# Performance work log

Measured on AMD Instinct MI355X. Metric: run time of the kernel, lower is better.

The kernel has to match this reference:

```python
import math
import jax, jax.numpy as jnp
import numpy as np

N_HEAD = 1
NORM_GROUPS = 32
EPS = 1e-5


def setup_inputs() -> dict:
    key = jax.random.key(0)
    ks = jax.random.split(key, 3)
    B, C, H, W, L = 4, 64, 16, 16, 16
    x = jax.random.normal(ks[0], (B, C, H, W, L), dtype=jnp.float32)
    gn_weight = jnp.ones((C,), dtype=jnp.float32)
    gn_bias = jnp.zeros((C,), dtype=jnp.float32)
    # 1x1x1 conv == per-voxel matmul; init like torch conv (kaiming-ish scale)
    qkv_weight = jax.random.normal(ks[1], (3 * C, C), dtype=jnp.float32) / math.sqrt(C)
    out_weight = jax.random.normal(ks[2], (C, C), dtype=jnp.float32) / math.sqrt(C)
    out_bias = jnp.zeros((C,), dtype=jnp.float32)
    return {"x": x, "gn_weight": gn_weight, "gn_bias": gn_bias,
            "qkv_weight": qkv_weight, "out_weight": out_weight, "out_bias": out_bias}


def _group_norm(x, w, b):
    B, C, H, W, L = x.shape
    g = NORM_GROUPS
    xg = x.reshape(B, g, C // g, H, W, L)
    mean = xg.mean(axis=(2, 3, 4, 5), keepdims=True)
    var = xg.var(axis=(2, 3, 4, 5), keepdims=True)
    xn = ((xg - mean) * jax.lax.rsqrt(var + EPS)).reshape(B, C, H, W, L)
    return xn * w[None, :, None, None, None] + b[None, :, None, None, None]


def reference(x, gn_weight, gn_bias, qkv_weight, out_weight, out_bias):
    B, C, H, W, L = x.shape
    n_head = N_HEAD
    head_dim = C // n_head
    N = H * W * L  # flattened voxel count

    norm = _group_norm(x, gn_weight, gn_bias)
    # 1x1x1 conv C -> 3C (no bias), then split heads
    qkv = jnp.einsum('bchwl,dc->bdhwl', norm, qkv_weight)
    qkv = qkv.reshape(B, n_head, 3 * head_dim, N)
    q, k, v = jnp.split(qkv, 3, axis=2)  # each [B, n_head, head_dim, N]

    # full N^2 attention; scale by sqrt(channel) as in the original (NOT head_dim)
    attn = jnp.einsum('bncq,bnck->bnqk', q, k) / math.sqrt(C)
    attn = jax.nn.softmax(attn, axis=-1)
    out = jnp.einsum('bnqk,bnck->bncq', attn, v).reshape(B, C, H, W, L)

    out = jnp.einsum('bchwl,dc->bdhwl', out, out_weight) + out_bias[None, :, None, None, None]
    return out + x
```

## Files before the change

### kernel.cpp

```cpp
#include <hip/hip_runtime.h>
#include <hip/hip_bf16.h>
#include <math.h>

#define BATCH 4
#define CH    64
#define NVOX  4096
#define NGRP  32
#define EPS   1e-5f
#define SPLITS 4
#define KVS   (NVOX / SPLITS)

typedef float f32x4 __attribute__((ext_vector_type(4)));
typedef short s16x8 __attribute__((ext_vector_type(8)));

static __device__ inline unsigned short f2bf(float f) {
    union { __hip_bfloat16 h; unsigned short u; } cv;
    cv.h = __float2bfloat16(f);
    return cv.u;
}

__global__ __launch_bounds__(256) void k_gnstats(const float* __restrict__ x,
                                                 float* __restrict__ stats) {
    int bg = blockIdx.x;
    const float4* p4 = (const float4*)(x + (size_t)bg * (2 * NVOX));
    float s = 0.f, sq = 0.f;
    for (int i = threadIdx.x; i < (2 * NVOX) / 4; i += 256) {
        float4 v = p4[i];
        s  += v.x + v.y + v.z + v.w;
        sq += v.x * v.x + v.y * v.y + v.z * v.z + v.w * v.w;
    }
    for (int off = 32; off; off >>= 1) {
        s  += __shfl_down(s, off);
        sq += __shfl_down(sq, off);
    }
    __shared__ float ls[4], lq[4];
    int wid = threadIdx.x >> 6;
    if ((threadIdx.x & 63) == 0) { ls[wid] = s; lq[wid] = sq; }
    __syncthreads();
    if (threadIdx.x == 0) {
        s  = ls[0] + ls[1] + ls[2] + ls[3];
        sq = lq[0] + lq[1] + lq[2] + lq[3];
        float mean = s / (float)(2 * NVOX);
        float var  = sq / (float)(2 * NVOX) - mean * mean;
        stats[bg]       = mean;
        stats[128 + bg] = rsqrtf(var + EPS);
    }
}

__global__ __launch_bounds__(256) void k_qkv(const float* __restrict__ x,
                                             const float* __restrict__ stats,
                                             const float* __restrict__ gw,
                                             const float* __restrict__ gb,
                                             const float* __restrict__ W,
                                             unsigned short* __restrict__ Qb,
                                             unsigned short* __restrict__ Kb,
                                             unsigned short* __restrict__ Vb) {
    int b  = blockIdx.x >> 6;
    int n0 = (blockIdx.x & 63) * 64;
    int t  = threadIdx.x;
    __shared__ float nm[64][64];
    __shared__ alignas(16) unsigned short tb[64][72];

    for (int i = t; i < 64 * 16; i += 256) {
        int c = i >> 4;
        int n = (i & 15) * 4;
        float4 v = *(const float4*)&x[((size_t)(b * CH + c)) * NVOX + n0 + n];
        float mean = stats[b * NGRP + (c >> 1)];
        float rstd = stats[128 + b * NGRP + (c >> 1)];
        float sc = rstd * gw[c];
        float sh = gb[c] - mean * sc;
        nm[c][n + 0] = v.x * sc + sh;
        nm[c][n + 1] = v.y * sc + sh;
        nm[c][n + 2] = v.z * sc + sh;
        nm[c][n + 3] = v.w * sc + sh;
    }
    __syncthreads();

    int nl = t & 63;
    int dg = t >> 6;
    float r[64];
    #pragma unroll
    for (int c = 0; c < 64; ++c) r[c] = nm[c][nl];

    #pragma unroll 4
    for (int j = 0; j < 16; ++j) {
        int d = dg * 16 + j;
        const float* w = &W[d * 64];
        float acc = 0.f;
        #pragma unroll
        for (int c = 0; c < 64; ++c) acc += w[c] * r[c];
        tb[nl][d] = f2bf(acc * 0.125f);
    }
    __syncthreads();
    {
        int n = t >> 2, d0 = (t & 3) * 16;
        s16x8 a0 = *(const s16x8*)&tb[n][d0];
        s16x8 a1 = *(const s16x8*)&tb[n][d0 + 8];
        size_t base = ((size_t)(b * NVOX + n0 + n)) * 64 + d0;
        *(s16x8*)&Qb[base]     = a0;
        *(s16x8*)&Qb[base + 8] = a1;
    }
    __syncthreads();

    #pragma unroll 4
    for (int j = 0; j < 16; ++j) {
        int d = dg * 16 + j;
        const float* w = &W[(64 + d) * 64];
        float acc = 0.f;
        #pragma unroll
        for (int c = 0; c < 64; ++c) acc += w[c] * r[c];
        tb[nl][d] = f2bf(acc);
    }
    __syncthreads();
    {
        int n = t >> 2, d0 = (t & 3) * 16;
        s16x8 a0 = *(const s16x8*)&tb[n][d0];
        s16x8 a1 = *(const s16x8*)&tb[n][d0 + 8];
        size_t base = ((size_t)(b * NVOX + n0 + n)) * 64 + d0;
        *(s16x8*)&Kb[base]     = a0;
        *(s16x8*)&Kb[base + 8] = a1;
    }

    #pragma unroll 4
    for (int j = 0; j < 16; ++j) {
        int d = dg * 16 + j;
        const float* w = &W[(128 + d) * 64];
        float acc = 0.f;
        #pragma unroll
        for (int c = 0; c < 64; ++c) acc += w[c] * r[c];
        Vb[((size_t)(b * 64 + d)) * NVOX + n0 + nl] = f2bf(acc);
    }
}

__global__ __launch_bounds__(256) void k_attn(const unsigned short* __restrict__ Qb,
                                              const unsigned short* __restrict__ Kb,
                                              const unsigned short* __restrict__ Vb,
                                              float* __restrict__ Opart,
                                              float* __restrict__ Mpart,
                                              float* __restrict__ Lpart) {
    int split = blockIdx.x & 3;
    int bq    = blockIdx.x >> 2;
    int b     = bq >> 6;
    int q0    = (bq & 63) * 64;
    int t     = threadIdx.x;
    int lane  = t & 63;
    int w     = t >> 6;
    const int kbase = split * KVS;

    __shared__ alignas(16) unsigned short Ks[64][72];
    __shared__ alignas(16) unsigned short Vs[64][72];
    __shared__ alignas(16) unsigned short Ps[4][16][72];

    const unsigned short* Qp = Qb + (size_t)b * NVOX * 64;
    const unsigned short* Kp = Kb + (size_t)b * NVOX * 64;
    const unsigned short* Vp = Vb + (size_t)b * 64 * NVOX;

    int l15 = lane & 15;
    int g4  = lane >> 4;
    int csl = g4 * 8;
    int qrow = q0 + w * 16 + l15;
    s16x8 qf0 = *(const s16x8*)&Qp[(size_t)qrow * 64 + csl];
    s16x8 qf1 = *(const s16x8*)&Qp[(size_t)qrow * 64 + csl + 32];

    f32x4 acc_o[4] = {};
    float m_r[4], l_r[4];
    #pragma unroll
    for (int i = 0; i < 4; ++i) { m_r[i] = -1e30f; l_r[i] = 0.f; }

    int sr = t >> 2;
    int sc = (t & 3) * 16;

    s16x8 kr0, kr1, vr0, vr1;
    {
        const s16x8* pk = (const s16x8*)&Kp[((size_t)(kbase + sr)) * 64 + sc];
        kr0 = pk[0]; kr1 = pk[1];
        const s16x8* pv = (const s16x8*)&Vp[(size_t)sr * NVOX + kbase + sc];
        vr0 = pv[0]; vr1 = pv[1];
    }

    for (int it = 0; it < KVS / 64; ++it) {
        *(s16x8*)&Ks[sr][sc]     = kr0;
        *(s16x8*)&Ks[sr][sc + 8] = kr1;
        *(s16x8*)&Vs[sr][sc]     = vr0;
        *(s16x8*)&Vs[sr][sc + 8] = vr1;
        __syncthreads();

        if (it < KVS / 64 - 1) {
            int k0n = kbase + (it + 1) * 64;
            const s16x8* pk = (const s16x8*)&Kp[((size_t)(k0n + sr)) * 64 + sc];
            kr0 = pk[0]; kr1 = pk[1];
            const s16x8* pv = (const s16x8*)&Vp[(size_t)sr * NVOX + k0n + sc];
            vr0 = pv[0]; vr1 = pv[1];
        }

        f32x4 sacc[4];
        #pragma unroll
        for (int kt = 0; kt < 4; ++kt) {
            s16x8 kf0 = *(const s16x8*)&Ks[kt * 16 + l15][csl];
            s16x8 kf1 = *(const s16x8*)&Ks[kt * 16 + l15][csl + 32];
            f32x4 z = {0.f, 0.f, 0.f, 0.f};
            sacc[kt] = __builtin_amdgcn_mfma_f32_16x16x32_bf16(qf0, kf0, z, 0, 0, 0);
            sacc[kt] = __builtin_amdgcn_mfma_f32_16x16x32_bf16(qf1, kf1, sacc[kt], 0, 0, 0);
        }

        float al[4];
        #pragma unroll
        for (int reg = 0; reg < 4; ++reg) {
            float rmax = fmaxf(fmaxf(sacc[0][reg], sacc[1][reg]),
                               fmaxf(sacc[2][reg], sacc[3][reg]));
            rmax = fmaxf(rmax, __shfl_xor(rmax, 1));
            rmax = fmaxf(rmax, __shfl_xor(rmax, 2));
            rmax = fmaxf(rmax, __shfl_xor(rmax, 4));
            rmax = fmaxf(rmax, __shfl_xor(rmax, 8));
            float mn = fmaxf(m_r[reg], rmax);
            al[reg] = __expf(m_r[reg] - mn);
            m_r[reg] = mn;
        }
        float p[4][4];
        #pragma unroll
        for (int kt = 0; kt < 4; ++kt)
            #pragma unroll
            for (int reg = 0; reg < 4; ++reg)
                p[kt][reg] = __expf(sacc[kt][reg] - m_r[reg]);
        #pragma unroll
        for (int reg = 0; reg < 4; ++reg) {
            float rs = p[0][reg] + p[1][reg] + p[2][reg] + p[3][reg];
            rs += __shfl_xor(rs, 1);
            rs += __shfl_xor(rs, 2);
            rs += __shfl_xor(rs, 4);
            rs += __shfl_xor(rs, 8);
            l_r[reg] = l_r[reg] * al[reg] + rs;
        }
        #pragma unroll
        for (int kt = 0; kt < 4; ++kt)
            #pragma unroll
            for (int reg = 0; reg < 4; ++reg)
                Ps[w][g4 * 4 + reg][kt * 16 + l15] = f2bf(p[kt][reg]);
        #pragma unroll
        for (int ct = 0; ct < 4; ++ct)
            #pragma unroll
            for (int reg = 0; reg < 4; ++reg)
                acc_o[ct][reg] *= al[reg];

        s16x8 pf0 = *(const s16x8*)&Ps[w][l15][csl];
        s16x8 pf1 = *(const s16x8*)&Ps[w][l15][csl + 32];
        #pragma unroll
        for (int ct = 0; ct < 4; ++ct) {
            s16x8 vf0 = *(const s16x8*)&Vs[ct * 16 + l15][csl];
            s16x8 vf1 = *(const s16x8*)&Vs[ct * 16 + l15][csl + 32];
            acc_o[ct] = __builtin_amdgcn_mfma_f32_16x16x32_bf16(pf0, vf0, acc_o[ct], 0, 0, 0);
            acc_o[ct] = __builtin_amdgcn_mfma_f32_16x16x32_bf16(pf1, vf1, acc_o[ct], 0, 0, 0);
        }
        __syncthreads();
    }

    #pragma unroll
    for (int ct = 0; ct < 4; ++ct)
        #pragma unroll
        for (int reg = 0; reg < 4; ++reg) {
            int q = q0 + w * 16 + g4 * 4 + reg;
            Opart[(((size_t)split * BATCH + b) * NVOX + q) * 64 + ct * 16 + l15] =
                acc_o[ct][reg];
        }
    if (l15 == 0) {
        #pragma unroll
        for (int reg = 0; reg < 4; ++reg) {
            int q = q0 + w * 16 + g4 * 4 + reg;
            Mpart[((size_t)split * BATCH + b) * NVOX + q] = m_r[reg];
            Lpart[((size_t)split * BATCH + b) * NVOX + q] = l_r[reg];
        }
    }
}

__global__ __launch_bounds__(256) void k_outproj(const float* __restrict__ Opart,
                                                 const float* __restrict__ Mpart,
                                                 const float* __restrict__ Lpart,
                                                 const float* __restrict__ Wout,
                                                 const float* __restrict__ obias,
                                                 const float* __restrict__ x,
                                                 float* __restrict__ out) {
    int b  = blockIdx.x >> 6;
    int n0 = (blockIdx.x & 63) * 64;
    int t  = threadIdx.x;
    __shared__ float os[64][65];
    __shared__ float scs[64][4];

    if (t < 64) {
        size_t qg = (size_t)b * NVOX + n0 + t;
        float m[SPLITS], l[SPLITS];
        #pragma unroll
        for (int s = 0; s < SPLITS; ++s) {
            m[s] = Mpart[(size_t)s * BATCH * NVOX + qg];
            l[s] = Lpart[(size_t)s * BATCH * NVOX + qg];
        }
        float mm = fmaxf(fmaxf(m[0], m[1]), fmaxf(m[2], m[3]));
        float e[SPLITS], lsum = 0.f;
        #pragma unroll
        for (int s = 0; s < SPLITS; ++s) { e[s] = __expf(m[s] - mm); lsum += l[s] * e[s]; }
        float inv = 1.f / lsum;
        #pragma unroll
        for (int s = 0; s < SPLITS; ++s) scs[t][s] = e[s] * inv;
    }
    __syncthreads();

    for (int i = t; i < 64 * 16; i += 256) {
        int n  = i >> 4;
        int c4 = (i & 15) * 4;
        size_t base = ((size_t)(b * NVOX + n0 + n)) * 64 + c4;
        float4 a = {0.f, 0.f, 0.f, 0.f};
        #pragma unroll
        for (int s = 0; s < SPLITS; ++s) {
            float4 v = *(const float4*)&Opart[(size_t)s * BATCH * NVOX * 64 + base];
            float f = scs[n][s];
            a.x += f * v.x; a.y += f * v.y; a.z += f * v.z; a.w += f * v.w;
        }
        os[n][c4 + 0] = a.x; os[n][c4 + 1] = a.y;
        os[n][c4 + 2] = a.z; os[n][c4 + 3] = a.w;
    }
    __syncthreads();

    int nl = t & 63;
    int dg = t >> 6;
    float r[64];
    #pragma unroll
    for (int c = 0; c < 64; ++c) r[c] = os[nl][c];
    #pragma unroll 4
    for (int j = 0; j < 16; ++j) {
        int d = dg * 16 + j;
        const float* wv = &Wout[d * 64];
        float acc = obias[d];
        #pragma unroll
        for (int c = 0; c < 64; ++c) acc += wv[c] * r[c];
        size_t idx = ((size_t)(b * CH + d)) * NVOX + n0 + nl;
        out[idx] = acc + x[idx];
    }
}

extern "C" void kernel_launch(void* const* d_in, const int* in_sizes, int n_in,
                              void* d_out, int out_size, void* d_ws, size_t ws_size,
                              hipStream_t stream) {
    const float* x     = (const float*)d_in[0];
    const float* gw    = (const float*)d_in[1];
    const float* gb    = (const float*)d_in[2];
    const float* Wqkv  = (const float*)d_in[3];
    const float* Wout  = (const float*)d_in[4];
    const float* obias = (const float*)d_in[5];
    float* out = (float*)d_out;

    float* ws    = (float*)d_ws;
    float* stats = ws;
    unsigned short* Qb = (unsigned short*)(ws + 256);
    unsigned short* Kb = Qb + (size_t)BATCH * NVOX * 64;
    unsigned short* Vb = Kb + (size_t)BATCH * NVOX * 64;
    float* Opart = (float*)(Vb + (size_t)BATCH * NVOX * 64);
    float* Mpart = Opart + (size_t)SPLITS * BATCH * NVOX * 64;
    float* Lpart = Mpart + (size_t)SPLITS * BATCH * NVOX;

    k_gnstats<<<BATCH * NGRP,        256, 0, stream>>>(x, stats);
    k_qkv   <<<BATCH * 64,           256, 0, stream>>>(x, stats, gw, gb, Wqkv, Qb, Kb, Vb);
    k_attn  <<<BATCH * 64 * SPLITS,  256, 0, stream>>>(Qb, Kb, Vb, Opart, Mpart, Lpart);
    k_outproj<<<BATCH * 64,          256, 0, stream>>>(Opart, Mpart, Lpart, Wout, obias, x, out);
}
```

Before: 190.7 us.

## Compute QKV projection with bf16 MFMA instead of scalar FP32 dot products

The QKV projection kernel now stages the projection weights and the normalized activations as bf16 in shared memory. Each wave computes 16 output channels for Q, K and V using 16x16x32 bf16 MFMA instructions, replacing the per-thread scalar 64-wide FP32 dot products. The aim is to cut ALU cost and the intermediate shared-memory transposes and barriers. In exchange, the activations and weights lose precision to bf16 before the matmul, and every block reloads and converts the whole weight matrix.

```diff
diff --git a/kernel.cpp b/kernel.cpp
--- a/kernel.cpp
+++ b/kernel.cpp
@@ -12,6 +12,7 @@
 
 typedef float f32x4 __attribute__((ext_vector_type(4)));
 typedef short s16x8 __attribute__((ext_vector_type(8)));
+typedef unsigned short u16x4 __attribute__((ext_vector_type(4)));
 
 static __device__ inline unsigned short f2bf(float f) {
     union { __hip_bfloat16 h; unsigned short u; } cv;
@@ -58,77 +59,66 @@
     int b  = blockIdx.x >> 6;
     int n0 = (blockIdx.x & 63) * 64;
     int t  = threadIdx.x;
-    __shared__ float nm[64][64];
-    __shared__ alignas(16) unsigned short tb[64][72];
-
+    __shared__ alignas(16) unsigned short Wl[192][72];
+    __shared__ alignas(16) unsigned short nt[64][72];
+
+    for (int i = t; i < 192 * 16; i += 256) {
+        int d  = i >> 4;
+        int c4 = (i & 15) * 4;
+        float4 v = *(const float4*)&W[d * 64 + c4];
+        u16x4 p = { f2bf(v.x), f2bf(v.y), f2bf(v.z), f2bf(v.w) };
+        *(u16x4*)&Wl[d][c4] = p;
+    }
     for (int i = t; i < 64 * 16; i += 256) {
-        int c = i >> 4;
-        int n = (i & 15) * 4;
-        float4 v = *(const float4*)&x[((size_t)(b * CH + c)) * NVOX + n0 + n];
+        int c  = i >> 4;
+        int n4 = (i & 15) * 4;
+        float4 v = *(const float4*)&x[((size_t)(b * CH + c)) * NVOX + n0 + n4];
         float mean = stats[b * NGRP + (c >> 1)];
         float rstd = stats[128 + b * NGRP + (c >> 1)];
         float sc = rstd * gw[c];
         float sh = gb[c] - mean * sc;
-        nm[c][n + 0] = v.x * sc + sh;
-        nm[c][n + 1] = v.y * sc + sh;
-        nm[c][n + 2] = v.z * sc + sh;
-        nm[c][n + 3] = v.w * sc + sh;
+        nt[n4 + 0][c] = f2bf(v.x * sc + sh);
+        nt[n4 + 1][c] = f2bf(v.y * sc + sh);
+        nt[n4 + 2][c] = f2bf(v.z * sc + sh);
+        nt[n4 + 3][c] = f2bf(v.w * sc + sh);
     }
     __syncthreads();
 
-    int nl = t & 63;
-    int dg = t >> 6;
-    float r[64];
+    int lane = t & 63;
+    int w    = t >> 6;
+    int l15  = lane & 15;
+    int g4   = lane >> 4;
+    int csl  = g4 * 8;
+
+    s16x8 aQ0 = *(const s16x8*)&Wl[      w * 16 + l15][csl];
+    s16x8 aQ1 = *(const s16x8*)&Wl[      w * 16 + l15][csl + 32];
+    s16x8 aK0 = *(const s16x8*)&Wl[ 64 + w * 16 + l15][csl];
+    s16x8 aK1 = *(const s16x8*)&Wl[ 64 + w * 16 + l15][csl + 32];
+    s16x8 aV0 = *(const s16x8*)&Wl[128 + w * 16 + l15][csl];
+    s16x8 aV1 = *(const s16x8*)&Wl[128 + w * 16 + l15][csl + 32];
+
     #pragma unroll
-    for (int c = 0; c < 64; ++c) r[c] = nm[c][nl];
-
-    #pragma unroll 4
-    for (int j = 0; j < 16; ++j) {
-        int d = dg * 16 + j;
-        const float* w = &W[d * 64];
-        float acc = 0.f;
-        #pragma unroll
-        for (int c = 0; c < 64; ++c) acc += w[c] * r[c];
-        tb[nl][d] = f2bf(acc * 0.125f);
-    }
-    __syncthreads();
-    {
-        int n = t >> 2, d0 = (t & 3) * 16;
-        s16x8 a0 = *(const s16x8*)&tb[n][d0];
-        s16x8 a1 = *(const s16x8*)&tb[n][d0 + 8];
-        size_t base = ((size_t)(b * NVOX + n0 + n)) * 64 + d0;
-        *(s16x8*)&Qb[base]     = a0;
-        *(s16x8*)&Qb[base + 8] = a1;
-    }
-    __syncthreads();
-
-    #pragma unroll 4
-    for (int j = 0; j < 16; ++j) {
-        int d = dg * 16 + j;
-        const float* w = &W[(64 + d) * 64];
-        float acc = 0.f;
-        #pragma unroll
-        for (int c = 0; c < 64; ++c) acc += w[c] * r[c];
-        tb[nl][d] = f2bf(acc);
-    }
-    __syncthreads();
-    {
-        int n = t >> 2, d0 = (t & 3) * 16;
-        s16x8 a0 = *(const s16x8*)&tb[n][d0];
-        s16x8 a1 = *(const s16x8*)&tb[n][d0 + 8];
-        size_t base = ((size_t)(b * NVOX + n0 + n)) * 64 + d0;
-        *(s16x8*)&Kb[base]     = a0;
-        *(s16x8*)&Kb[base + 8] = a1;
-    }
-
-    #pragma unroll 4
-    for (int j = 0; j < 16; ++j) {
-        int d = dg * 16 + j;
-        const float* w = &W[(128 + d) * 64];
-        float acc = 0.f;
-        #pragma unroll
-        for (int c = 0; c < 64; ++c) acc += w[c] * r[c];
-        Vb[((size_t)(b * 64 + d)) * NVOX + n0 + nl] = f2bf(acc);
+    for (int nti = 0; nti < 4; ++nti) {
+        s16x8 b0 = *(const s16x8*)&nt[nti * 16 + l15][csl];
+        s16x8 b1 = *(const s16x8*)&nt[nti * 16 + l15][csl + 32];
+        f32x4 z = {0.f, 0.f, 0.f, 0.f};
+        f32x4 dq = __builtin_amdgcn_mfma_f32_16x16x32_bf16(aQ0, b0, z, 0, 0, 0);
+        dq = __builtin_amdgcn_mfma_f32_16x16x32_bf16(aQ1, b1, dq, 0, 0, 0);
+        f32x4 dk = __builtin_amdgcn_mfma_f32_16x16x32_bf16(aK0, b0, z, 0, 0, 0);
+        dk = __builtin_amdgcn_mfma_f32_16x16x32_bf16(aK1, b1, dk, 0, 0, 0);
+        f32x4 dv = __builtin_amdgcn_mfma_f32_16x16x32_bf16(aV0, b0, z, 0, 0, 0);
+        dv = __builtin_amdgcn_mfma_f32_16x16x32_bf16(aV1, b1, dv, 0, 0, 0);
+
+        int n = n0 + nti * 16 + l15;
+        u16x4 pq = { f2bf(dq[0] * 0.125f), f2bf(dq[1] * 0.125f),
+                     f2bf(dq[2] * 0.125f), f2bf(dq[3] * 0.125f) };
+        u16x4 pk = { f2bf(dk[0]), f2bf(dk[1]), f2bf(dk[2]), f2bf(dk[3]) };
+        size_t qkbase = ((size_t)(b * NVOX + n)) * 64 + w * 16 + g4 * 4;
+        *(u16x4*)&Qb[qkbase] = pq;
+        *(u16x4*)&Kb[qkbase] = pk;
+        #pragma unroll
+        for (int reg = 0; reg < 4; ++reg)
+            Vb[((size_t)(b * 64 + w * 16 + g4 * 4 + reg)) * NVOX + n] = f2bf(dv[reg]);
     }
 }
 
```

After: 159.6 us. 1.19x faster.
